# Performance work log

Hardware: AMD Instinct MI355X
Metric: run time of the kernel (lower is better)

The kernel has to match this reference:

```python
import jax, jax.numpy as jnp
import numpy as np

B, S, D = 8, 8192, 512
E, DFF = 16, 512
CAPACITY = 2


def setup_inputs() -> dict:
    key = jax.random.key(0)
    ks = jax.random.split(key, 4)
    x = jax.random.normal(ks[0], (B, S, D), dtype=jnp.float32)
    gate_weight = jax.random.normal(ks[1], (D, E), dtype=jnp.float32) * 0.006
    w1 = jax.random.normal(ks[2], (E, D, DFF), dtype=jnp.float32) * 0.02
    b1 = jnp.zeros((E, DFF), dtype=jnp.float32)
    w2 = jax.random.normal(ks[3], (E, DFF, D), dtype=jnp.float32) * 0.02
    b2 = jnp.zeros((E, D), dtype=jnp.float32)
    return {"x": x, "gate_weight": gate_weight, "w1": w1, "b1": b1, "w2": w2, "b2": b2}


def reference(x, gate_weight, w1, b1, w2, b2):
    Bx, Sx, Dx = x.shape
    num_experts = gate_weight.shape[1]
    k = Sx // num_experts * CAPACITY  # tokens per expert (capacity limit)

    # Router: softmax over experts, then each expert picks its top-k tokens.
    logits = jnp.einsum('bsd,de->bse', x, gate_weight)
    affinity = jax.nn.softmax(logits, axis=-1).transpose(0, 2, 1)  # [b, e, s]
    gating, index = jax.lax.top_k(affinity, k)  # [b, e, k] each

    # Dispatch: gather selected tokens per expert (== one-hot einsum in torch).
    x_in = jnp.take_along_axis(x[:, None, :, :], index[..., None], axis=2)  # [b, e, k, d]

    # Per-expert MLP (grouped GEMM over expert axis).
    h = jax.nn.gelu(jnp.einsum('bekd,edh->bekh', x_in, w1) + b1[None, :, None, :])
    x_e = jnp.einsum('bekh,ehd->bekd', h, w2) + b2[None, :, None, :]

    # Combine: weight by gate prob and scatter-add back to token positions.
    weighted = gating[..., None] * x_e  # [b, e, k, d]
    out = jnp.zeros_like(x)
    idx_flat = index.reshape(Bx, num_experts * k)
    vals_flat = weighted.reshape(Bx, num_experts * k, Dx)
    out = out.at[jnp.arange(Bx)[:, None], idx_flat].add(vals_flat)
    return out
```

## Files before the change

### kernel.cpp

```cpp
#include <hip/hip_runtime.h>
#include <hip/hip_bf16.h>

typedef __attribute__((ext_vector_type(8))) short short8;
typedef __attribute__((ext_vector_type(4))) float floatx4;
typedef __attribute__((ext_vector_type(4))) unsigned short ushort4_t;

#define B_    8
#define S_    8192
#define D_    512
#define E_    16
#define DFF_  512
#define KROW_ 1024

__device__ __forceinline__ float bf2f(unsigned short u) {
    return __uint_as_float(((unsigned int)u) << 16);
}
__device__ __forceinline__ unsigned short f2bf(float f) {
    unsigned int u = __float_as_uint(f);
    u += 0x7FFFu + ((u >> 16) & 1u);
    return (unsigned short)(u >> 16);
}
__device__ __forceinline__ float gelu_tanh(float v) {
    const float t = v * fmaf(0.0713548065f, v * v, 1.5957691216057308f);
    return v * __builtin_amdgcn_rcpf(1.0f + __expf(-t));
}

#define GLD16(g, l) __builtin_amdgcn_global_load_lds( \
    (const __attribute__((address_space(1))) void*)(g), \
    (__attribute__((address_space(3))) void*)(l), 16, 0, 0)

__global__ __launch_bounds__(256) void cvt_x_k(
    const float* __restrict__ x, unsigned short* __restrict__ xb, int n8)
{
    int i = blockIdx.x * 256 + threadIdx.x;
    if (i >= n8) return;
    float4 va = ((const float4*)x)[2 * i];
    float4 vb = ((const float4*)x)[2 * i + 1];
    short8 o;
    o[0] = (short)f2bf(va.x); o[1] = (short)f2bf(va.y);
    o[2] = (short)f2bf(va.z); o[3] = (short)f2bf(va.w);
    o[4] = (short)f2bf(vb.x); o[5] = (short)f2bf(vb.y);
    o[6] = (short)f2bf(vb.z); o[7] = (short)f2bf(vb.w);
    ((short8*)xb)[i] = o;
}

__global__ __launch_bounds__(256) void transpose_w_k(
    const float* __restrict__ w1, const float* __restrict__ w2,
    unsigned short* __restrict__ w1t, unsigned short* __restrict__ w2t)
{
    __shared__ unsigned short tile[32][33];
    const int e = blockIdx.z & 15;
    const float*    src = (blockIdx.z < 16) ? w1 : w2;
    unsigned short* dst = (blockIdx.z < 16) ? w1t : w2t;
    const int x0 = blockIdx.x * 32, y0 = blockIdx.y * 32;
    const int tx = threadIdx.x, ty = threadIdx.y;
    const size_t base = (size_t)e * 512 * 512;
#pragma unroll
    for (int i = 0; i < 4; ++i)
        tile[ty + 8 * i][tx] = f2bf(src[base + (size_t)(y0 + ty + 8 * i) * 512 + x0 + tx]);
    __syncthreads();
#pragma unroll
    for (int i = 0; i < 4; ++i)
        dst[base + (size_t)(x0 + ty + 8 * i) * 512 + y0 + tx] = tile[tx][ty + 8 * i];
}

__global__ __launch_bounds__(512) void router_k(
    const float* __restrict__ x,
    const float* __restrict__ gw,
    float* __restrict__ aff)
{
    __shared__ float gws[D_ * E_];
    const int t = threadIdx.x;
    for (int i = t; i < D_ * E_; i += 512) gws[i] = gw[i];
    __syncthreads();

    const int lane = t & 63;
    const int sub  = lane & 7;
    const int tok  = blockIdx.x * 64 + (t >> 3);
    const float4* xr = (const float4*)(x + (size_t)tok * D_);

    float acc0 = 0.f, acc1 = 0.f;
#pragma unroll 4
    for (int d8 = 0; d8 < D_ / 8; ++d8) {
        const float4 va = xr[2 * d8];
        const float4 vb = xr[2 * d8 + 1];
#pragma unroll
        for (int q = 0; q < 8; ++q) {
            const float xv = (q < 4) ? (&va.x)[q] : (&vb.x)[q - 4];
            const float2 gv = *(const float2*)&gws[(d8 * 8 + q) * E_ + 2 * sub];
            acc0 = fmaf(xv, gv.x, acc0);
            acc1 = fmaf(xv, gv.y, acc1);
        }
    }

    const int base = lane & 56;
    float accs[E_];
#pragma unroll
    for (int i = 0; i < 8; ++i) {
        accs[2 * i]     = __shfl(acc0, base + i);
        accs[2 * i + 1] = __shfl(acc1, base + i);
    }
    float mx = accs[0];
#pragma unroll
    for (int e = 1; e < E_; ++e) mx = fmaxf(mx, accs[e]);
    const float e0v = expf(acc0 - mx);
    const float e1v = expf(acc1 - mx);
    float sm = 0.f;
#pragma unroll
    for (int i = 0; i < 8; ++i) {
        sm += __shfl(e0v, base + i);
        sm += __shfl(e1v, base + i);
    }
    const float inv = 1.f / sm;
    const int b = tok >> 13, s = tok & (S_ - 1);
    aff[((size_t)b * E_ + 2 * sub) * S_ + s]     = e0v * inv;
    aff[((size_t)b * E_ + 2 * sub + 1) * S_ + s] = e1v * inv;
}

__global__ __launch_bounds__(1024) void topk_k(
    const float* __restrict__ aff, int* __restrict__ idxb, int* __restrict__ map)
{
    __shared__ unsigned int keys[S_];
    __shared__ unsigned int hist[4][257];
    __shared__ unsigned int wsum[16];
    __shared__ unsigned int sh_b, sh_above, sh_ctr;

    const int b = blockIdx.x >> 4, e = blockIdx.x & 15;
    const float* a = aff + ((size_t)b * E_ + e) * S_;
    const int t = threadIdx.x;
    const int lane = t & 63, wid = t >> 6;

    for (int i = t; i < S_; i += 1024) keys[i] = __float_as_uint(a[i]);
    if (t == 0) sh_ctr = 0;
    hist[t >> 8][t & 255] = 0;
    __syncthreads();

    unsigned int prefix = 0, need = KROW_;
#pragma unroll
    for (int lev = 0; lev < 4; ++lev) {
        const int shift = (lev == 0) ? 23 : (lev == 1) ? 15 : (lev == 2) ? 7 : 0;
        const unsigned int fmask = (lev == 3) ? 127u : 255u;
        const int sw = shift + ((lev == 3) ? 7 : 8);
        const unsigned int mask_hi = 0xFFFFFFFFu << sw;

        for (int i = t; i < S_; i += 1024) {
            unsigned int k = keys[i];
            if ((k & mask_hi) == prefix)
                atomicAdd(&hist[t >> 8][(k >> shift) & fmask], 1u);
        }
        __syncthreads();

        if (t < 64) {
            unsigned int s0 = 0, s1 = 0, s2 = 0, s3 = 0;
#pragma unroll
            for (int c = 0; c < 4; ++c) {
                s0 += hist[c][4 * t + 0]; s1 += hist[c][4 * t + 1];
                s2 += hist[c][4 * t + 2]; s3 += hist[c][4 * t + 3];
            }
            const unsigned int v3 = s3, v2 = s2 + v3, v1 = s1 + v2, v0 = s0 + v1;
            const unsigned int G = v0;
            unsigned int T = v0;
#pragma unroll
            for (int off = 1; off < 64; off <<= 1) {
                unsigned int u = (unsigned int)__shfl_down((int)T, off);
                if (lane + off < 64) T += u;
            }
            const unsigned int R = T - G;
            unsigned int Sv[5];
            Sv[0] = T; Sv[1] = v1 + R; Sv[2] = v2 + R; Sv[3] = v3 + R; Sv[4] = R;
#pragma unroll
            for (int k2 = 0; k2 < 4; ++k2)
                if (Sv[k2] >= need && Sv[k2 + 1] < need) {
                    sh_b = (unsigned int)(4 * t + k2);
                    sh_above = Sv[k2 + 1];
                }
        }
        __syncthreads();
        prefix |= sh_b << shift;
        need   -= sh_above;
        if (lev < 3) hist[t >> 8][t & 255] = 0;
        __syncthreads();
    }

    const unsigned int thr = prefix;
    const unsigned int need_eq = need;
    const unsigned int m_gt = KROW_ - need_eq;

    int* idxg = idxb + ((size_t)b * E_ + e) * KROW_;
    for (int i = t; i < S_; i += 1024) {
        unsigned int k = keys[i];
        if (k > thr) {
            unsigned int slot = atomicAdd(&sh_ctr, 1u);
            idxg[slot] = i;
            map[((size_t)b * S_ + i) * E_ + e] = (int)slot;
        }
    }
    unsigned int lt = 0;
    const int i0 = t * 8;
#pragma unroll
    for (int q = 0; q < 8; ++q) lt += (keys[i0 + q] == thr);
    unsigned int incl = lt;
#pragma unroll
    for (int off = 1; off < 64; off <<= 1) {
        unsigned int u = (unsigned int)__shfl_up((int)incl, off);
        if (lane >= off) incl += u;
    }
    if (lane == 63) wsum[wid] = incl;
    __syncthreads();
    if (t < 16) {
        unsigned int wv = wsum[t];
        unsigned int ex = wv;
#pragma unroll
        for (int off = 1; off < 16; off <<= 1) {
            unsigned int u = (unsigned int)__shfl_up((int)ex, off);
            if (lane >= off) ex += u;
        }
        wsum[t] = ex - wv;
    }
    __syncthreads();
    unsigned int r = (incl - lt) + wsum[wid];
#pragma unroll
    for (int q = 0; q < 8; ++q) {
        if (keys[i0 + q] == thr) {
            if (r < need_eq) {
                idxg[m_gt + r] = i0 + q;
                map[((size_t)b * S_ + (i0 + q)) * E_ + e] = (int)(m_gt + r);
            }
            r++;
        }
    }
}

__global__ __launch_bounds__(256) void gemm1_k(
    const unsigned short* __restrict__ xb,
    const unsigned short* __restrict__ w1t,
    const float* __restrict__ b1,
    const int* __restrict__ idxb,
    unsigned short* __restrict__ h,
    int b_base)
{
    __shared__ unsigned short As[2][128 * 32];
    __shared__ unsigned short Bs[2][128 * 32];
    const int e  = blockIdx.z & 15;
    const int bl = blockIdx.z >> 4;
    const int b  = b_base + bl;
    const int m0 = blockIdx.x * 128;
    const int n0 = blockIdx.y * 128;
    const int t = threadIdx.x;
    const int w = t >> 6, l = t & 63;
    const int r0 = t >> 2, c0 = (t & 3) * 8;

    const int* idxg = idxb + ((size_t)b * E_ + e) * KROW_;
    const int s0 = idxg[m0 + r0];
    const int s1 = idxg[m0 + 64 + r0];
    const unsigned short* a0 = xb + ((size_t)b * S_ + s0) * D_ + c0;
    const unsigned short* a1 = xb + ((size_t)b * S_ + s1) * D_ + c0;
    const unsigned short* g0 = w1t + ((size_t)e * DFF_ + n0 + r0) * D_ + c0;
    const unsigned short* g1 = w1t + ((size_t)e * DFF_ + n0 + 64 + r0) * D_ + c0;

    floatx4 acc[4][4];
#pragma unroll
    for (int i = 0; i < 4; ++i)
#pragma unroll
        for (int j = 0; j < 4; ++j) acc[i][j] = (floatx4){0.f, 0.f, 0.f, 0.f};

    const int wm = (w >> 1) * 64, wn = (w & 1) * 64;
    const int lane15 = l & 15, lk = (l >> 4) * 8;

    {
        unsigned short* asd = &As[0][w * 512];
        unsigned short* bsd = &Bs[0][w * 512];
        GLD16(a0, asd); GLD16(a1, asd + 2048);
        GLD16(g0, bsd); GLD16(g1, bsd + 2048);
    }
    __syncthreads();

#pragma unroll
    for (int kt = 0; kt < D_ / 32; ++kt) {
        const int cur = kt & 1;
        if (kt + 1 < D_ / 32) {
            const int k1 = (kt + 1) * 32;
            unsigned short* asd = &As[cur ^ 1][w * 512];
            unsigned short* bsd = &Bs[cur ^ 1][w * 512];
            GLD16(a0 + k1, asd); GLD16(a1 + k1, asd + 2048);
            GLD16(g0 + k1, bsd); GLD16(g1 + k1, bsd + 2048);
        }
        short8 af[4], bf[4];
#pragma unroll
        for (int i = 0; i < 4; ++i) af[i] = *(const short8*)&As[cur][(wm + i * 16 + lane15) * 32 + lk];
#pragma unroll
        for (int j = 0; j < 4; ++j) bf[j] = *(const short8*)&Bs[cur][(wn + j * 16 + lane15) * 32 + lk];
#pragma unroll
        for (int i = 0; i < 4; ++i)
#pragma unroll
            for (int j = 0; j < 4; ++j)
                acc[i][j] = __builtin_amdgcn_mfma_f32_16x16x32_bf16(af[i], bf[j], acc[i][j], 0, 0, 0);
        __syncthreads();
    }

    float biasv[4];
#pragma unroll
    for (int j = 0; j < 4; ++j) biasv[j] = b1[e * DFF_ + n0 + wn + j * 16 + lane15];

    const size_t hbase = ((size_t)bl * E_ + e) * KROW_ * DFF_;
#pragma unroll
    for (int i = 0; i < 4; ++i)
#pragma unroll
        for (int j = 0; j < 4; ++j) {
            const int n = n0 + wn + j * 16 + lane15;
#pragma unroll
            for (int r = 0; r < 4; ++r) {
                const int m = m0 + wm + i * 16 + (l >> 4) * 4 + r;
                h[hbase + (size_t)m * DFF_ + n] = f2bf(gelu_tanh(acc[i][j][r] + biasv[j]));
            }
        }
}

__global__ __launch_bounds__(256) void gemm2_k(
    const unsigned short* __restrict__ h,
    const unsigned short* __restrict__ w2t,
    const float* __restrict__ b2,
    unsigned short* __restrict__ ex)
{
    __shared__ unsigned short As[2][128 * 32];
    __shared__ unsigned short Bs[2][128 * 32];
    const int e  = blockIdx.z & 15;
    const int bl = blockIdx.z >> 4;
    const int m0 = blockIdx.x * 128;
    const int n0 = blockIdx.y * 128;
    const int t = threadIdx.x;
    const int w = t >> 6, l = t & 63;
    const int r0 = t >> 2, c0 = (t & 3) * 8;

    const unsigned short* a0 = h + (((size_t)bl * E_ + e) * KROW_ + m0 + r0) * DFF_ + c0;
    const unsigned short* a1 = h + (((size_t)bl * E_ + e) * KROW_ + m0 + 64 + r0) * DFF_ + c0;
    const unsigned short* g0 = w2t + ((size_t)e * D_ + n0 + r0) * DFF_ + c0;
    const unsigned short* g1 = w2t + ((size_t)e * D_ + n0 + 64 + r0) * DFF_ + c0;

    floatx4 acc[4][4];
#pragma unroll
    for (int i = 0; i < 4; ++i)
#pragma unroll
        for (int j = 0; j < 4; ++j) acc[i][j] = (floatx4){0.f, 0.f, 0.f, 0.f};

    const int wm = (w >> 1) * 64, wn = (w & 1) * 64;
    const int lane15 = l & 15, lk = (l >> 4) * 8;

    {
        unsigned short* asd = &As[0][w * 512];
        unsigned short* bsd = &Bs[0][w * 512];
        GLD16(a0, asd); GLD16(a1, asd + 2048);
        GLD16(g0, bsd); GLD16(g1, bsd + 2048);
    }
    __syncthreads();

#pragma unroll
    for (int kt = 0; kt < DFF_ / 32; ++kt) {
        const int cur = kt & 1;
        if (kt + 1 < DFF_ / 32) {
            const int k1 = (kt + 1) * 32;
            unsigned short* asd = &As[cur ^ 1][w * 512];
            unsigned short* bsd = &Bs[cur ^ 1][w * 512];
            GLD16(a0 + k1, asd); GLD16(a1 + k1, asd + 2048);
            GLD16(g0 + k1, bsd); GLD16(g1 + k1, bsd + 2048);
        }
        short8 af[4], bf[4];
#pragma unroll
        for (int i = 0; i < 4; ++i) af[i] = *(const short8*)&As[cur][(wm + i * 16 + lane15) * 32 + lk];
#pragma unroll
        for (int j = 0; j < 4; ++j) bf[j] = *(const short8*)&Bs[cur][(wn + j * 16 + lane15) * 32 + lk];
#pragma unroll
        for (int i = 0; i < 4; ++i)
#pragma unroll
            for (int j = 0; j < 4; ++j)
                acc[i][j] = __builtin_amdgcn_mfma_f32_16x16x32_bf16(af[i], bf[j], acc[i][j], 0, 0, 0);
        __syncthreads();
    }

    float biasv[4];
#pragma unroll
    for (int j = 0; j < 4; ++j) biasv[j] = b2[e * D_ + n0 + wn + j * 16 + lane15];

    const size_t xbase = ((size_t)bl * E_ + e) * KROW_ * D_;
#pragma unroll
    for (int i = 0; i < 4; ++i)
#pragma unroll
        for (int j = 0; j < 4; ++j) {
            const int n = n0 + wn + j * 16 + lane15;
#pragma unroll
            for (int r = 0; r < 4; ++r) {
                const int m = m0 + wm + i * 16 + (l >> 4) * 4 + r;
                ex[xbase + (size_t)m * D_ + n] = f2bf(acc[i][j][r] + biasv[j]);
            }
        }
}

__global__ __launch_bounds__(256) void combine_k(
    const unsigned short* __restrict__ ex, const float* __restrict__ aff,
    const int* __restrict__ map, float* __restrict__ out, int b_base)
{
    const int t = threadIdx.x;
    const int w = t >> 6, l = t & 63;
    const size_t tokl = (size_t)blockIdx.x * 4 + w;
    const int bl = (int)(tokl >> 13);
    const int s  = (int)(tokl & (S_ - 1));
    const int b  = b_base + bl;

    int jv = -1; float gv = 0.f;
    if (l < 16) {
        jv = map[((size_t)b * S_ + s) * E_ + l];
        gv = aff[((size_t)b * E_ + l) * S_ + s];
    }
    float acc[8] = {0.f, 0.f, 0.f, 0.f, 0.f, 0.f, 0.f, 0.f};
#pragma unroll
    for (int e = 0; e < E_; ++e) {
        const int je = __shfl(jv, e);
        if (je < 0) continue;
        const float ge = __shfl(gv, e);
        const unsigned short* row = ex + (((size_t)bl * E_ + e) * KROW_ + je) * D_ + l * 8;
        short8 v = *(const short8*)row;
#pragma unroll
        for (int q = 0; q < 8; ++q) acc[q] += ge * bf2f((unsigned short)v[q]);
    }
    float* orow = out + ((size_t)b * S_ + s) * D_ + l * 8;
    float4 o0 = {acc[0], acc[1], acc[2], acc[3]};
    float4 o1 = {acc[4], acc[5], acc[6], acc[7]};
    ((float4*)orow)[0] = o0;
    ((float4*)orow)[1] = o1;
}

extern "C" void kernel_launch(void* const* d_in, const int* in_sizes, int n_in,
                              void* d_out, int out_size, void* d_ws, size_t ws_size,
                              hipStream_t stream) {
    const float* x  = (const float*)d_in[0];
    const float* gw = (const float*)d_in[1];
    const float* w1 = (const float*)d_in[2];
    const float* b1 = (const float*)d_in[3];
    const float* w2 = (const float*)d_in[4];
    const float* b2 = (const float*)d_in[5];
    float* out = (float*)d_out;
    char* ws = (char*)d_ws;

    size_t off = 0;
    float* aff = (float*)(ws + off);          off += (size_t)B_ * E_ * S_ * 4;
    int* idxb  = (int*)(ws + off);            off += (size_t)B_ * E_ * KROW_ * 4;
    int* map   = (int*)(ws + off);            off += (size_t)B_ * S_ * E_ * 4;
    unsigned short* w1t = (unsigned short*)(ws + off); off += (size_t)E_ * DFF_ * D_ * 2;
    unsigned short* w2t = (unsigned short*)(ws + off); off += (size_t)E_ * D_ * DFF_ * 2;
    unsigned short* xb  = (unsigned short*)(ws + off); off += (size_t)B_ * S_ * D_ * 2;
    const size_t fixed = off;
    const size_t per_b_h  = (size_t)E_ * KROW_ * DFF_ * 2;
    const size_t per_b_ex = (size_t)E_ * KROW_ * D_ * 2;
    const size_t per_b = per_b_h + per_b_ex;

    int bchunk = 1;
    if (ws_size > fixed + per_b) {
        size_t m = (ws_size - fixed) / per_b;
        bchunk = (int)(m > (size_t)B_ ? (size_t)B_ : m);
        if (bchunk < 1) bchunk = 1;
    }
    unsigned short* h  = (unsigned short*)(ws + fixed);
    unsigned short* ex = (unsigned short*)(ws + fixed + (size_t)bchunk * per_b_h);

    hipMemsetAsync(map, 0xFF, (size_t)B_ * S_ * E_ * 4, stream);
    cvt_x_k<<<dim3((B_ * S_ * D_ / 8 + 255) / 256), dim3(256), 0, stream>>>(
        x, xb, B_ * S_ * D_ / 8);
    transpose_w_k<<<dim3(16, 16, 32), dim3(32, 8, 1), 0, stream>>>(w1, w2, w1t, w2t);
    router_k<<<dim3((B_ * S_) / 64), dim3(512), 0, stream>>>(x, gw, aff);
    topk_k<<<dim3(B_ * E_), dim3(1024), 0, stream>>>(aff, idxb, map);

    for (int b0 = 0; b0 < B_; b0 += bchunk) {
        const int bc = (b0 + bchunk <= B_) ? bchunk : (B_ - b0);
        gemm1_k<<<dim3(KROW_ / 128, DFF_ / 128, bc * E_), dim3(256), 0, stream>>>(
            xb, w1t, b1, idxb, h, b0);
        gemm2_k<<<dim3(KROW_ / 128, D_ / 128, bc * E_), dim3(256), 0, stream>>>(
            h, w2t, b2, ex);
        combine_k<<<dim3(bc * (S_ / 4)), dim3(256), 0, stream>>>(ex, aff, map, out, b0);
    }
}
```

Baseline: 605.0 us.

## Remap GEMM workgroups across XCDs by expert and privatize top-k histograms per wave

Both grouped GEMM kernels now compute tile coordinates from a remapped linear workgroup id. Consecutive tiles of the same expert and batch then land on the same XCD, so they share expert weights and gathered rows in that XCD's L2. The top-k radix-select kernel widens its shared histogram from 4 to 16 copies, one per wavefront, to cut LDS atomic contention. In exchange, zeroing and summing the histograms costs more per level. The remap hardcodes 8 M-tiles, 4 N-tiles and 8 XCDs.

```diff
diff --git a/kernel.cpp b/kernel.cpp
--- a/kernel.cpp
+++ b/kernel.cpp
@@ -28,6 +28,19 @@
 #define GLD16(g, l) __builtin_amdgcn_global_load_lds( \
     (const __attribute__((address_space(1))) void*)(g), \
     (__attribute__((address_space(3))) void*)(l), 16, 0, 0)
+
+__device__ __forceinline__ void xcd_remap(int& m0i, int& n0i, int& bl, int& e) {
+    const int total = (int)(gridDim.x * gridDim.y * gridDim.z);
+    const int chunk = total >> 3;
+    const int wgid  = (int)(blockIdx.x + gridDim.x * (blockIdx.y + gridDim.y * blockIdx.z));
+    const int widx  = (wgid & 7) * chunk + (wgid >> 3);
+    n0i = widx & 3;
+    m0i = (widx >> 2) & 7;
+    const int tz  = widx >> 5;
+    const int nbl = (int)(gridDim.z >> 4);
+    bl = tz % nbl;
+    e  = tz / nbl;
+}
 
 __global__ __launch_bounds__(256) void cvt_x_k(
     const float* __restrict__ x, unsigned short* __restrict__ xb, int n8)
@@ -121,7 +134,7 @@
     const float* __restrict__ aff, int* __restrict__ idxb, int* __restrict__ map)
 {
     __shared__ unsigned int keys[S_];
-    __shared__ unsigned int hist[4][257];
+    __shared__ unsigned int hist[16][257];
     __shared__ unsigned int wsum[16];
     __shared__ unsigned int sh_b, sh_above, sh_ctr;
 
@@ -132,7 +145,7 @@
 
     for (int i = t; i < S_; i += 1024) keys[i] = __float_as_uint(a[i]);
     if (t == 0) sh_ctr = 0;
-    hist[t >> 8][t & 255] = 0;
+    for (int i = t; i < 16 * 257; i += 1024) ((unsigned int*)hist)[i] = 0;
     __syncthreads();
 
     unsigned int prefix = 0, need = KROW_;
@@ -146,14 +159,14 @@
         for (int i = t; i < S_; i += 1024) {
             unsigned int k = keys[i];
             if ((k & mask_hi) == prefix)
-                atomicAdd(&hist[t >> 8][(k >> shift) & fmask], 1u);
+                atomicAdd(&hist[wid][(k >> shift) & fmask], 1u);
         }
         __syncthreads();
 
         if (t < 64) {
             unsigned int s0 = 0, s1 = 0, s2 = 0, s3 = 0;
 #pragma unroll
-            for (int c = 0; c < 4; ++c) {
+            for (int c = 0; c < 16; ++c) {
                 s0 += hist[c][4 * t + 0]; s1 += hist[c][4 * t + 1];
                 s2 += hist[c][4 * t + 2]; s3 += hist[c][4 * t + 3];
             }
@@ -178,7 +191,9 @@
         __syncthreads();
         prefix |= sh_b << shift;
         need   -= sh_above;
-        if (lev < 3) hist[t >> 8][t & 255] = 0;
+        if (lev < 3) {
+            for (int i = t; i < 16 * 257; i += 1024) ((unsigned int*)hist)[i] = 0;
+        }
         __syncthreads();
     }
 
@@ -241,11 +256,11 @@
 {
     __shared__ unsigned short As[2][128 * 32];
     __shared__ unsigned short Bs[2][128 * 32];
-    const int e  = blockIdx.z & 15;
-    const int bl = blockIdx.z >> 4;
+    int m0i, n0i, bl, e;
+    xcd_remap(m0i, n0i, bl, e);
     const int b  = b_base + bl;
-    const int m0 = blockIdx.x * 128;
-    const int n0 = blockIdx.y * 128;
+    const int m0 = m0i * 128;
+    const int n0 = n0i * 128;
     const int t = threadIdx.x;
     const int w = t >> 6, l = t & 63;
     const int r0 = t >> 2, c0 = (t & 3) * 8;
@@ -324,10 +339,10 @@
 {
     __shared__ unsigned short As[2][128 * 32];
     __shared__ unsigned short Bs[2][128 * 32];
-    const int e  = blockIdx.z & 15;
-    const int bl = blockIdx.z >> 4;
-    const int m0 = blockIdx.x * 128;
-    const int n0 = blockIdx.y * 128;
+    int m0i, n0i, bl, e;
+    xcd_remap(m0i, n0i, bl, e);
+    const int m0 = m0i * 128;
+    const int n0 = n0i * 128;
     const int t = threadIdx.x;
     const int w = t >> 6, l = t & 63;
     const int r0 = t >> 2, c0 = (t & 3) * 8;
```

Result: faster. 573.9 us (-5.1%).
